# Performance work log

Hardware: AMD Instinct MI355X
Metric: run time of the kernel (lower is better)

## Reference

```python
import jax, jax.numpy as jnp
import numpy as np

TEMPERATURE = 0.07
EPS = 1e-12  # F.normalize eps
DIAG_FILL = -10.0


def _l1_normalize(x):
    # F.normalize(x, p=1, dim=-1): x / max(sum|x|, eps)
    denom = jnp.maximum(jnp.sum(jnp.abs(x), axis=-1, keepdims=True), EPS)
    return x / denom


def setup_inputs() -> dict:
    key = jax.random.key(0)
    k1, k2 = jax.random.split(key)
    B, D, H, W = 4, 128, 64, 64
    feat_q = jax.random.normal(k1, (B, D, H, W), dtype=jnp.float32)
    feat_k = jax.random.normal(k2, (B, D, H, W), dtype=jnp.float32)
    return {"feat_q": feat_q, "feat_k": feat_k}


def reference(feat_q, feat_k):
    B, D = feat_q.shape[0], feat_q.shape[1]
    # [B, D, H, W] -> [B, N, D]
    q = feat_q.reshape(B, D, -1).transpose(0, 2, 1)
    k = feat_k.reshape(B, D, -1).transpose(0, 2, 1)
    q = _l1_normalize(q)
    k = _l1_normalize(k)
    k = jax.lax.stop_gradient(k)  # feat_k.detach()
    N = q.shape[1]
    # similarity matrix [B, N, N]
    sim = jnp.einsum('bnd,bmd->bnm', q, k)
    eye = jnp.eye(N, dtype=bool)
    sim = jnp.where(eye[None, :, :], DIAG_FILL, sim)
    logits = sim.reshape(-1, N) / TEMPERATURE  # negatives
    # out = concat([zeros, logits]); CE with target 0 => loss row = logsumexp(out) - 0
    lse = jax.nn.logsumexp(logits, axis=-1)
    loss = jnp.mean(jnp.logaddexp(jnp.float32(0.0), lse))
    return loss
```

## Files before the change

### kernel.cpp

```cpp
#include <hip/hip_runtime.h>

#define NB 4
#define DD 128
#define NN 4096
#define EXP2C 20.60992915555662f

typedef __attribute__((ext_vector_type(8))) short bf16x8;
typedef __attribute__((ext_vector_type(4))) float f32x4;

static __device__ __forceinline__ unsigned short f32_to_bf16(float x){
  unsigned u = __float_as_uint(x);
  u += 0x7fffu + ((u >> 16) & 1u);
  return (unsigned short)(u >> 16);
}

static __device__ __forceinline__ void async_copy16(const uint4* g, uint4* l){
  __builtin_amdgcn_global_load_lds(
      (const __attribute__((address_space(1))) unsigned int*)g,
      (__attribute__((address_space(3))) unsigned int*)l, 16, 0, 0);
}

__global__ __launch_bounds__(256) void norm_kernel(const float* __restrict__ fq,
                                                   const float* __restrict__ fk,
                                                   unsigned short* __restrict__ qn,
                                                   unsigned short* __restrict__ kn,
                                                   float* __restrict__ rowsum,
                                                   float* __restrict__ out){
  const float* src = blockIdx.z ? fk : fq;
  unsigned short* dst = blockIdx.z ? kn : qn;
  int b = blockIdx.y;
  int n0 = blockIdx.x * 64;
  int t = threadIdx.x;
  if (blockIdx.z == 0 && t < 64) rowsum[b*NN + n0 + t] = 0.f;
  if (blockIdx.z == 0 && blockIdx.x == 0 && b == 0 && t == 64) *out = 0.f;
  __shared__ float sT[64][129];
  __shared__ float red[4][64];
  __shared__ float srd[64];
  const float* sb = src + (size_t)b*DD*NN + n0;
  #pragma unroll
  for (int it = 0; it < 8; ++it){
    int idx = it*256 + t;
    int d = idx >> 4, g = idx & 15;
    const float4 v = *reinterpret_cast<const float4*>(sb + (size_t)d*NN + g*4);
    sT[g*4+0][d] = v.x;
    sT[g*4+1][d] = v.y;
    sT[g*4+2][d] = v.z;
    sT[g*4+3][d] = v.w;
  }
  __syncthreads();
  {
    int nn = t & 63, part = t >> 6;
    float s = 0.f;
    #pragma unroll
    for (int j = 0; j < 32; ++j) s += fabsf(sT[nn][part*32 + j]);
    red[part][nn] = s;
  }
  __syncthreads();
  if (t < 64){
    float dsum = red[0][t] + red[1][t] + red[2][t] + red[3][t];
    float r = 1.f / fmaxf(dsum, 1e-12f);
    srd[t] = blockIdx.z ? r : r * EXP2C;
  }
  __syncthreads();
  unsigned short* db = dst + ((size_t)b*NN + n0)*DD;
  #pragma unroll
  for (int it = 0; it < 4; ++it){
    int c = it*256 + t;
    int row = c >> 4, dc = c & 15;
    float r = srd[row];
    unsigned v[4];
    #pragma unroll
    for (int p = 0; p < 4; ++p){
      unsigned short lo = f32_to_bf16(sT[row][dc*8 + p*2    ] * r);
      unsigned short hi = f32_to_bf16(sT[row][dc*8 + p*2 + 1] * r);
      v[p] = (unsigned)lo | ((unsigned)hi << 16);
    }
    uint4 pack = make_uint4(v[0], v[1], v[2], v[3]);
    int sw = dc ^ (row & 15);
    *reinterpret_cast<uint4*>(db + (size_t)row*DD + sw*8) = pack;
  }
}

__global__ __launch_bounds__(256) void simexp_kernel(const unsigned short* __restrict__ qn,
                                                     const unsigned short* __restrict__ kn,
                                                     float* __restrict__ rowsum){
  __shared__ uint4 sK[2][1024];
  int t = threadIdx.x;
  int w = t >> 6, lane = t & 63;
  int quad = lane >> 4, l16 = lane & 15;
  int b  = blockIdx.z;
  int r0 = blockIdx.x * 128;
  int c0 = blockIdx.y * 256;
  const uint4* gq = reinterpret_cast<const uint4*>(qn + ((size_t)b*NN + r0)*DD);
  const uint4* gk = reinterpret_cast<const uint4*>(kn + ((size_t)b*NN + c0)*DD);
  #pragma unroll
  for (int i = 0; i < 4; ++i)
    async_copy16(gk + w*256 + i*64 + lane, &sK[0][w*256 + i*64]);
  bf16x8 a[2][4];
  #pragma unroll
  for (int i = 0; i < 2; ++i){
    int rbase = (w*32 + i*16 + l16) * 16;
    #pragma unroll
    for (int ks = 0; ks < 4; ++ks)
      a[i][ks] = __builtin_bit_cast(bf16x8, gq[rbase + ((ks*4 + quad) ^ l16)]);
  }
  float rsum[8];
  #pragma unroll
  for (int s = 0; s < 8; ++s) rsum[s] = 0.f;
  __syncthreads();

  #pragma unroll
  for (int kt = 0; kt < 4; ++kt){
    const int cur = kt & 1;
    if (kt < 3){
      #pragma unroll
      for (int i = 0; i < 4; ++i)
        async_copy16(gk + (kt+1)*1024 + w*256 + i*64 + lane, &sK[cur^1][w*256 + i*64]);
    }
    f32x4 acc[2][4];
    #pragma unroll
    for (int i = 0; i < 2; ++i)
      #pragma unroll
      for (int j = 0; j < 4; ++j)
        acc[i][j] = (f32x4){0.f, 0.f, 0.f, 0.f};
    #pragma unroll
    for (int ks = 0; ks < 4; ++ks){
      bf16x8 bfr[4];
      #pragma unroll
      for (int j = 0; j < 4; ++j)
        bfr[j] = __builtin_bit_cast(bf16x8, sK[cur][(j*16 + l16)*16 + ((ks*4 + quad) ^ l16)]);
      #pragma unroll
      for (int i = 0; i < 2; ++i)
        #pragma unroll
        for (int j = 0; j < 4; ++j)
          acc[i][j] = __builtin_amdgcn_mfma_f32_16x16x32_bf16(a[i][ks], bfr[j], acc[i][j], 0, 0, 0);
    }
    {
      int g = c0 + kt*64 - r0;
      if (g == 0 || g == 64){
        bool hit = (quad == (l16 >> 2));
        int rr = l16 & 3;
        int jb = 2*w - (g >> 4);
        #pragma unroll
        for (int i = 0; i < 2; ++i){
          int jd = jb + i;
          if (jd >= 0 && jd < 4){
            #pragma unroll
            for (int r = 0; r < 4; ++r)
              acc[i][jd][r] = (hit && r == rr) ? -1e38f : acc[i][jd][r];
          }
        }
      }
    }
    #pragma unroll
    for (int i = 0; i < 2; ++i)
      #pragma unroll
      for (int j = 0; j < 4; ++j)
        #pragma unroll
        for (int r = 0; r < 4; ++r)
          rsum[i*4 + r] += exp2f(acc[i][j][r]);
    __syncthreads();
  }
  #pragma unroll
  for (int s = 0; s < 8; ++s){
    float v = rsum[s];
    v += __shfl_xor(v, 1, 64);
    v += __shfl_xor(v, 2, 64);
    v += __shfl_xor(v, 4, 64);
    v += __shfl_xor(v, 8, 64);
    if (l16 == 0){
      int row = r0 + w*32 + (s >> 2)*16 + quad*4 + (s & 3);
      atomicAdd(&rowsum[b*NN + row], v);
    }
  }
}

__global__ __launch_bounds__(256) void finalize_kernel(const float* __restrict__ rowsum,
                                                       float* __restrict__ out){
  int idx = blockIdx.x*256 + threadIdx.x;
  float loss = log1pf(rowsum[idx]);
  loss += __shfl_xor(loss, 1, 64);
  loss += __shfl_xor(loss, 2, 64);
  loss += __shfl_xor(loss, 4, 64);
  loss += __shfl_xor(loss, 8, 64);
  loss += __shfl_xor(loss, 16, 64);
  loss += __shfl_xor(loss, 32, 64);
  if ((threadIdx.x & 63) == 0)
    atomicAdd(out, loss * (1.f / (float)(NB*NN)));
}

extern "C" void kernel_launch(void* const* d_in, const int* in_sizes, int n_in,
                              void* d_out, int out_size, void* d_ws, size_t ws_size,
                              hipStream_t stream){
  const float* fq = (const float*)d_in[0];
  const float* fk = (const float*)d_in[1];
  unsigned short* qn = (unsigned short*)d_ws;
  unsigned short* kn = qn + (size_t)NB*NN*DD;
  float* rowsum = (float*)(kn + (size_t)NB*NN*DD);
  float* out = (float*)d_out;

  norm_kernel<<<dim3(NN/64, NB, 2), 256, 0, stream>>>(fq, fk, qn, kn, rowsum, out);
  simexp_kernel<<<dim3(NN/128, NN/256, NB), 256, 0, stream>>>(qn, kn, rowsum);
  finalize_kernel<<<dim3(NB*NN/256), 256, 0, stream>>>(rowsum, out);
}
```

Baseline: 111.7 us.

## Preload all K tiles into LDS, remap block order, use raw exp2

The sim kernel now issues all four K tile loads into a 64KB LDS buffer up front and drops the per-iteration double buffering and barrier. It also remaps the 1D grid so consecutive blocks land on different XCDs (block swizzle), raises wave priority around the MFMA section, disables unrolling of the outer loop, and uses the hardware exp2 builtin without range handling. The larger LDS footprint lowers how many blocks fit per CU, and the single upfront barrier waits for all loads before any compute starts.

```diff
diff --git a/kernel.cpp b/kernel.cpp
--- a/kernel.cpp
+++ b/kernel.cpp
@@ -7,6 +7,12 @@
 
 typedef __attribute__((ext_vector_type(8))) short bf16x8;
 typedef __attribute__((ext_vector_type(4))) float f32x4;
+
+#if __has_builtin(__builtin_amdgcn_exp2f)
+#define EXP2(x) __builtin_amdgcn_exp2f(x)
+#else
+#define EXP2(x) exp2f(x)
+#endif
 
 static __device__ __forceinline__ unsigned short f32_to_bf16(float x){
   unsigned u = __float_as_uint(x);
@@ -84,18 +90,15 @@
 __global__ __launch_bounds__(256) void simexp_kernel(const unsigned short* __restrict__ qn,
                                                      const unsigned short* __restrict__ kn,
                                                      float* __restrict__ rowsum){
-  __shared__ uint4 sK[2][1024];
+  __shared__ uint4 sK[4][1024];
   int t = threadIdx.x;
   int w = t >> 6, lane = t & 63;
   int quad = lane >> 4, l16 = lane & 15;
-  int b  = blockIdx.z;
-  int r0 = blockIdx.x * 128;
-  int c0 = blockIdx.y * 256;
+  int sw = (blockIdx.x & 7)*256 + (blockIdx.x >> 3);
+  int bx = sw & 31, by = (sw >> 5) & 15, bz = sw >> 9;
+  int b = bz, r0 = bx*128, c0 = by*256;
   const uint4* gq = reinterpret_cast<const uint4*>(qn + ((size_t)b*NN + r0)*DD);
   const uint4* gk = reinterpret_cast<const uint4*>(kn + ((size_t)b*NN + c0)*DD);
-  #pragma unroll
-  for (int i = 0; i < 4; ++i)
-    async_copy16(gk + w*256 + i*64 + lane, &sK[0][w*256 + i*64]);
   bf16x8 a[2][4];
   #pragma unroll
   for (int i = 0; i < 2; ++i){
@@ -104,37 +107,39 @@
     for (int ks = 0; ks < 4; ++ks)
       a[i][ks] = __builtin_bit_cast(bf16x8, gq[rbase + ((ks*4 + quad) ^ l16)]);
   }
+  #pragma unroll
+  for (int kt = 0; kt < 4; ++kt)
+    #pragma unroll
+    for (int i = 0; i < 4; ++i)
+      async_copy16(gk + kt*1024 + w*256 + i*64 + lane, &sK[kt][w*256 + i*64]);
+
   float rsum[8];
   #pragma unroll
   for (int s = 0; s < 8; ++s) rsum[s] = 0.f;
   __syncthreads();
 
-  #pragma unroll
+  #pragma unroll 1
   for (int kt = 0; kt < 4; ++kt){
-    const int cur = kt & 1;
-    if (kt < 3){
-      #pragma unroll
-      for (int i = 0; i < 4; ++i)
-        async_copy16(gk + (kt+1)*1024 + w*256 + i*64 + lane, &sK[cur^1][w*256 + i*64]);
-    }
     f32x4 acc[2][4];
     #pragma unroll
     for (int i = 0; i < 2; ++i)
       #pragma unroll
       for (int j = 0; j < 4; ++j)
         acc[i][j] = (f32x4){0.f, 0.f, 0.f, 0.f};
+    __builtin_amdgcn_s_setprio(1);
     #pragma unroll
     for (int ks = 0; ks < 4; ++ks){
       bf16x8 bfr[4];
       #pragma unroll
       for (int j = 0; j < 4; ++j)
-        bfr[j] = __builtin_bit_cast(bf16x8, sK[cur][(j*16 + l16)*16 + ((ks*4 + quad) ^ l16)]);
+        bfr[j] = __builtin_bit_cast(bf16x8, sK[kt][(j*16 + l16)*16 + ((ks*4 + quad) ^ l16)]);
       #pragma unroll
       for (int i = 0; i < 2; ++i)
         #pragma unroll
         for (int j = 0; j < 4; ++j)
           acc[i][j] = __builtin_amdgcn_mfma_f32_16x16x32_bf16(a[i][ks], bfr[j], acc[i][j], 0, 0, 0);
     }
+    __builtin_amdgcn_s_setprio(0);
     {
       int g = c0 + kt*64 - r0;
       if (g == 0 || g == 64){
@@ -158,8 +163,7 @@
       for (int j = 0; j < 4; ++j)
         #pragma unroll
         for (int r = 0; r < 4; ++r)
-          rsum[i*4 + r] += exp2f(acc[i][j][r]);
-    __syncthreads();
+          rsum[i*4 + r] += EXP2(acc[i][j][r]);
   }
   #pragma unroll
   for (int s = 0; s < 8; ++s){
@@ -200,6 +204,6 @@
   float* out = (float*)d_out;
 
   norm_kernel<<<dim3(NN/64, NB, 2), 256, 0, stream>>>(fq, fk, qn, kn, rowsum, out);
-  simexp_kernel<<<dim3(NN/128, NN/256, NB), 256, 0, stream>>>(qn, kn, rowsum);
+  simexp_kernel<<<dim3((NN/128)*(NN/256)*NB), 256, 0, stream>>>(qn, kn, rowsum);
   finalize_kernel<<<dim3(NB*NN/256), 256, 0, stream>>>(rowsum, out);
 }
```

After: 102.1 us. 1.09x faster.
